# Kernel tuning notes

Measured on AMD Instinct MI355X. Metric: run time of the kernel, lower is better.

Reference implementation:

```python
import jax, jax.numpy as jnp
import numpy as np

EPS = 1e-5
H, DH = 8, 8  # n_head, d_hidden


def setup_inputs() -> dict:
    key = jax.random.key(0)
    ks = jax.random.split(key, 6)
    B, N, L, D = 1, 512, 1024, 64
    s = 1.0 / np.sqrt(D)
    return {
        "msa": jax.random.normal(ks[0], (B, N, L, D), jnp.float32),
        "ln_w": jnp.ones((D,), jnp.float32),
        "ln_b": jnp.zeros((D,), jnp.float32),
        "Wq": jax.random.normal(ks[1], (D, H * DH), jnp.float32) * s,
        "Wk": jax.random.normal(ks[2], (D, DH), jnp.float32) * s,
        "Wv": jax.random.normal(ks[3], (D, DH), jnp.float32) * s,
        "Wg": jax.random.normal(ks[4], (D, H * DH), jnp.float32) * s,
        "bg": jnp.ones((H * DH,), jnp.float32),
        "Wout": jax.random.normal(ks[5], (D, D), jnp.float32) * s,
        "bout": jnp.zeros((D,), jnp.float32),
    }


def reference(msa, ln_w, ln_b, Wq, Wk, Wv, Wg, bg, Wout, bout):
    B, N, L, D = msa.shape
    # LayerNorm over d_msa
    mu = jnp.mean(msa, axis=-1, keepdims=True)
    var = jnp.mean(jnp.square(msa - mu), axis=-1, keepdims=True)
    x = (msa - mu) * jax.lax.rsqrt(var + EPS) * ln_w + ln_b

    # Global query: project, split heads, mean over the N (sequence) axis
    q = (x @ Wq).reshape(B, N, L, H, DH).mean(axis=1)  # (B, L, H, DH)
    k = x @ Wk  # (B, N, L, DH)
    v = x @ Wv  # (B, N, L, DH)
    gate = jax.nn.sigmoid(x @ Wg + bg)  # (B, N, L, H*DH)

    scale = 1.0 / np.sqrt(DH)
    # SDPA batched over (B, L): q_len = H, kv_len = N, head_dim = DH
    scores = jnp.einsum("blhd,bnld->blhn", q, k) * scale
    attn = jax.nn.softmax(scores, axis=-1)
    o = jnp.einsum("blhn,bnld->blhd", attn, v)  # (B, L, H, DH)
    o = o.reshape(B, 1, L, H * DH)  # broadcast over N via gate

    out = (gate * o) @ Wout + bout  # (B, N, L, D)
    return out
```

## Files before the change

### kernel.cpp

```cpp
#include <hip/hip_runtime.h>
#include <math.h>

#define DD 64
#define NN 512
#define LL 1024
#define EPSF 1e-5f
#define NCH 32

typedef short short8 __attribute__((ext_vector_type(8)));
typedef float f32x4 __attribute__((ext_vector_type(4)));

static __device__ __forceinline__ unsigned bf16_rne(float f) {
  unsigned u = __float_as_uint(f);
  return (u + 0x7FFFu + ((u >> 16) & 1u)) >> 16;
}
static __device__ __forceinline__ float bf16_hi_f(float f) {
  unsigned u = __float_as_uint(f);
  return __uint_as_float((u + 0x7FFFu + ((u >> 16) & 1u)) & 0xFFFF0000u);
}

__global__ __launch_bounds__(256) void kW(const float* __restrict__ Wg,
                                          const float* __restrict__ Wout,
                                          unsigned* __restrict__ Bpk)
{
  const int idx = blockIdx.x * 256 + threadIdx.x;
  const int e2   = idx & 3;
  const int lane = (idx >> 2) & 63;
  const int ctkt = (idx >> 8) & 7;
  const int h    = (idx >> 11) & 1;
  const int mv   = (idx >> 12) & 1;
  const int col  = ((ctkt >> 1) << 4) | (lane & 15);
  const int k0   = ((ctkt & 1) << 5) + ((lane >> 4) << 3) + (e2 << 1);
  const float* W = mv ? Wout : Wg;
  const float w0 = W[k0 * DD + col];
  const float w1 = W[(k0 + 1) * DD + col];
  unsigned b0, b1;
  if (h == 0) { b0 = bf16_rne(w0); b1 = bf16_rne(w1); }
  else        { b0 = bf16_rne(w0 - bf16_hi_f(w0)); b1 = bf16_rne(w1 - bf16_hi_f(w1)); }
  Bpk[idx] = b0 | (b1 << 16);
}

__global__ __launch_bounds__(256, 4) void kA(
    const float* __restrict__ msa, const float* __restrict__ lnw, const float* __restrict__ lnb,
    const float* __restrict__ Wk, const float* __restrict__ Wv,
    float* __restrict__ kb, float* __restrict__ vb, float* __restrict__ xbarP,
    unsigned short* __restrict__ xnh)
{
  __shared__ float xc[4][16][68];
  const int t = threadIdx.x;
  const int lane = t & 63;
  const int w = t >> 6;
  const int l_loc = t & 15;
  const int n_loc = t >> 4;
  const int lt = blockIdx.x & 63;
  const int nc = blockIdx.x >> 6;
  const int l0 = lt * 16;
  const int n = nc * 16 + n_loc;
  const int l = l0 + l_loc;

  float X[DD];
  {
    const float4* rp = (const float4*)(msa + ((size_t)n * LL + l) * DD);
#pragma unroll
    for (int i = 0; i < 16; ++i) {
      const float4 f = rp[i];
      X[4*i+0] = f.x; X[4*i+1] = f.y; X[4*i+2] = f.z; X[4*i+3] = f.w;
    }
  }

  float s = 0.f, s2 = 0.f;
#pragma unroll
  for (int d = 0; d < DD; ++d) { s += X[d]; s2 = fmaf(X[d], X[d], s2); }
  const float mu = s * (1.f / DD);
  const float rs = rsqrtf(fmaf(-mu, mu, s2 * (1.f / DD)) + EPSF);
  const float aa = rs, bb = -mu * rs;

  float ka[8], va[8];
#pragma unroll
  for (int j = 0; j < 8; ++j) { ka[j] = 0.f; va[j] = 0.f; }

  uint4* xg = (uint4*)xnh;
#pragma unroll
  for (int g = 0; g < 8; ++g) {
#pragma unroll
    for (int e = 0; e < 8; ++e) {
      const int d = 8 * g + e;
      const float xn = fmaf(fmaf(X[d], aa, bb), lnw[d], lnb[d]);
      X[d] = xn;
#pragma unroll
      for (int j = 0; j < 8; ++j) {
        ka[j] = fmaf(xn, Wk[d * 8 + j], ka[j]);
        va[j] = fmaf(xn, Wv[d * 8 + j], va[j]);
      }
    }
    uint4 q;
    q.x = bf16_rne(X[8*g+0]) | (bf16_rne(X[8*g+1]) << 16);
    q.y = bf16_rne(X[8*g+2]) | (bf16_rne(X[8*g+3]) << 16);
    q.z = bf16_rne(X[8*g+4]) | (bf16_rne(X[8*g+5]) << 16);
    q.w = bf16_rne(X[8*g+6]) | (bf16_rne(X[8*g+7]) << 16);
    xg[(size_t)(n * 8 + g) * LL + l] = q;
  }

  {
    float4* kp = (float4*)(kb + ((size_t)l * NN + n) * 8);
    float4* vp = (float4*)(vb + ((size_t)l * NN + n) * 8);
    kp[0] = make_float4(ka[0], ka[1], ka[2], ka[3]);
    kp[1] = make_float4(ka[4], ka[5], ka[6], ka[7]);
    vp[0] = make_float4(va[0], va[1], va[2], va[3]);
    vp[1] = make_float4(va[4], va[5], va[6], va[7]);
  }

  {
    const bool hi1 = (lane & 16) != 0;
#pragma unroll
    for (int k = 0; k < 32; ++k) {
      const float keep = hi1 ? X[k + 32] : X[k];
      const float send = hi1 ? X[k] : X[k + 32];
      X[k] = keep + __shfl_xor(send, 16);
    }
    const bool hi2 = (lane & 32) != 0;
#pragma unroll
    for (int k = 0; k < 16; ++k) {
      const float keep = hi2 ? X[k + 16] : X[k];
      const float send = hi2 ? X[k] : X[k + 16];
      X[k] = keep + __shfl_xor(send, 32);
    }
  }
  const int d0i = ((lane >> 4) & 1) * 32 + (lane >> 5) * 16;
#pragma unroll
  for (int k = 0; k < 16; ++k) xc[w][l_loc][d0i + k] = X[k];
  __syncthreads();

#pragma unroll
  for (int j = 0; j < 4; ++j) {
    const int c = t * 4 + j;
    const int ll = c >> 6, d = c & 63;
    const float sv = xc[0][ll][d] + xc[1][ll][d] + xc[2][ll][d] + xc[3][ll][d];
    xbarP[((size_t)(l0 + ll) * NCH + nc) * DD + d] = sv;
  }
}

__global__ __launch_bounds__(512) void kB(
    const float* __restrict__ kb, const float* __restrict__ vb,
    const float* __restrict__ xbarP, const float* __restrict__ Wq,
    float* __restrict__ obT)
{
  __shared__ float xbL[DD];
  __shared__ float qs[DD];
  __shared__ float ks[NN * 9];
  __shared__ float vs[NN * 9];
  const int l = blockIdx.x;
  const int t = threadIdx.x;
  const int h = t >> 6;
  const int lane = t & 63;

  const float* kl = kb + (size_t)l * NN * 8;
  const float* vl = vb + (size_t)l * NN * 8;
#pragma unroll
  for (int i = 0; i < 8; ++i) {
    const int idx = i * 512 + t;
    const int n = idx >> 3, j = idx & 7;
    ks[n*9 + j] = kl[idx];
    vs[n*9 + j] = vl[idx];
  }
  if (t < DD) {
    float s = 0.f;
    for (int p = 0; p < NCH; ++p) s += xbarP[((size_t)l * NCH + p) * DD + t];
    xbL[t] = s * (1.f / NN);
  }
  __syncthreads();
  if (t < DD) {
    float acc = 0.f;
    for (int d = 0; d < DD; ++d) acc = fmaf(xbL[d], Wq[d*DD + t], acc);
    qs[t] = acc * 0.35355339059327373f;
  }
  __syncthreads();

  float sc[8];
  float m = -1e30f;
#pragma unroll
  for (int i = 0; i < 8; ++i) {
    const int n = i * 64 + lane;
    float s = 0.f;
#pragma unroll
    for (int d = 0; d < 8; ++d) s = fmaf(qs[h*8 + d], ks[n*9 + d], s);
    sc[i] = s;
    m = fmaxf(m, s);
  }
#pragma unroll
  for (int off = 32; off; off >>= 1) m = fmaxf(m, __shfl_xor(m, off));
  float ssum = 0.f;
#pragma unroll
  for (int i = 0; i < 8; ++i) { sc[i] = __expf(sc[i] - m); ssum += sc[i]; }
#pragma unroll
  for (int off = 32; off; off >>= 1) ssum += __shfl_xor(ssum, off);
  const float inv = 1.f / ssum;

  float oacc[8];
#pragma unroll
  for (int d = 0; d < 8; ++d) oacc[d] = 0.f;
#pragma unroll
  for (int i = 0; i < 8; ++i) {
    const int n = i * 64 + lane;
#pragma unroll
    for (int d = 0; d < 8; ++d) oacc[d] = fmaf(sc[i], vs[n*9 + d], oacc[d]);
  }
#pragma unroll
  for (int d = 0; d < 8; ++d) {
#pragma unroll
    for (int off = 32; off; off >>= 1) oacc[d] += __shfl_xor(oacc[d], off);
  }
  if (lane == 0) {
#pragma unroll
    for (int d = 0; d < 8; ++d)
      obT[(size_t)(h * 8 + d) * LL + l] = oacc[d] * inv;
  }
}

__global__ __launch_bounds__(256, 4) void kC(
    const unsigned short* __restrict__ xnh, const unsigned* __restrict__ Bpk,
    const float* __restrict__ bg, const float* __restrict__ obT,
    const float* __restrict__ bout, float* __restrict__ out)
{
  __shared__ unsigned short TH[128 * 72];
  __shared__ unsigned short TL[128 * 72];
  const int t = threadIdx.x;
  const int lane = t & 63;
  const int w = t >> 6;
  const int rbase = 32 * w;
  const size_t R0 = (size_t)blockIdx.x * 128;
  const int nblk = (int)(R0 >> 10);
  const int lbase = (int)(R0 & (LL - 1));

  const short8* Bp = (const short8*)Bpk;
  const short8* Xp = (const short8*)xnh;

  f32x4 acc[2][4];
#pragma unroll
  for (int rt = 0; rt < 2; ++rt)
#pragma unroll
    for (int ct = 0; ct < 4; ++ct) acc[rt][ct] = f32x4{0.f, 0.f, 0.f, 0.f};

  {
    short8 ah[2][2];
#pragma unroll
    for (int rt = 0; rt < 2; ++rt) {
      const int ar_l = lbase + rbase + rt * 16 + (lane & 15);
      const int g = lane >> 4;
      ah[rt][0] = Xp[(size_t)(nblk * 8 + g) * LL + ar_l];
      ah[rt][1] = Xp[(size_t)(nblk * 8 + 4 + g) * LL + ar_l];
    }
#pragma unroll
    for (int ct = 0; ct < 4; ++ct) {
      const short8 bh0 = Bp[(0 * 8 + ct * 2 + 0) * 64 + lane];
      const short8 bh1 = Bp[(0 * 8 + ct * 2 + 1) * 64 + lane];
      const short8 bl0 = Bp[(1 * 8 + ct * 2 + 0) * 64 + lane];
      const short8 bl1 = Bp[(1 * 8 + ct * 2 + 1) * 64 + lane];
#pragma unroll
      for (int rt = 0; rt < 2; ++rt) {
        f32x4 c = acc[rt][ct];
        c = __builtin_amdgcn_mfma_f32_16x16x32_bf16(ah[rt][0], bh0, c, 0, 0, 0);
        c = __builtin_amdgcn_mfma_f32_16x16x32_bf16(ah[rt][1], bh1, c, 0, 0, 0);
        c = __builtin_amdgcn_mfma_f32_16x16x32_bf16(ah[rt][0], bl0, c, 0, 0, 0);
        c = __builtin_amdgcn_mfma_f32_16x16x32_bf16(ah[rt][1], bl1, c, 0, 0, 0);
        acc[rt][ct] = c;
      }
    }
  }

#pragma unroll
  for (int rt = 0; rt < 2; ++rt) {
    const int rl0 = rbase + rt * 16 + ((lane >> 4) << 2);
    const int li0 = (int)((R0 + rl0) & (LL - 1));
#pragma unroll
    for (int ct = 0; ct < 4; ++ct) {
      const int col = ct * 16 + (lane & 15);
      const float4 ov = *(const float4*)&obT[(size_t)col * LL + li0];
      const float bgc = bg[col];
#define SIG_STORE(j, ocomp)                                             \
      {                                                                 \
        const float pre = acc[rt][ct][j] + bgc;                         \
        const float tv = (ocomp) / (1.f + __expf(-pre));                \
        const unsigned hb = bf16_rne(tv);                               \
        TH[(rl0 + (j)) * 72 + col] = (unsigned short)hb;                \
        const float rvl = tv - __uint_as_float(hb << 16);               \
        TL[(rl0 + (j)) * 72 + col] = (unsigned short)bf16_rne(rvl);     \
      }
      SIG_STORE(0, ov.x) SIG_STORE(1, ov.y) SIG_STORE(2, ov.z) SIG_STORE(3, ov.w)
#undef SIG_STORE
    }
  }

#pragma unroll
  for (int rt = 0; rt < 2; ++rt)
#pragma unroll
    for (int ct = 0; ct < 4; ++ct) {
      const float bo = bout[ct * 16 + (lane & 15)];
      acc[rt][ct] = f32x4{bo, bo, bo, bo};
    }
  {
    short8 ah[2][2], al[2][2];
#pragma unroll
    for (int rt = 0; rt < 2; ++rt) {
      const int ar = rbase + rt * 16 + (lane & 15);
      const int kg = (lane >> 4) * 8;
      ah[rt][0] = *(const short8*)&TH[ar * 72 + kg];
      ah[rt][1] = *(const short8*)&TH[ar * 72 + 32 + kg];
      al[rt][0] = *(const short8*)&TL[ar * 72 + kg];
      al[rt][1] = *(const short8*)&TL[ar * 72 + 32 + kg];
    }
#pragma unroll
    for (int ct = 0; ct < 4; ++ct) {
      const short8 bh0 = Bp[(2 * 8 + ct * 2 + 0) * 64 + lane];
      const short8 bh1 = Bp[(2 * 8 + ct * 2 + 1) * 64 + lane];
      const short8 bl0 = Bp[(3 * 8 + ct * 2 + 0) * 64 + lane];
      const short8 bl1 = Bp[(3 * 8 + ct * 2 + 1) * 64 + lane];
#pragma unroll
      for (int rt = 0; rt < 2; ++rt) {
        f32x4 c = acc[rt][ct];
        c = __builtin_amdgcn_mfma_f32_16x16x32_bf16(ah[rt][0], bh0, c, 0, 0, 0);
        c = __builtin_amdgcn_mfma_f32_16x16x32_bf16(ah[rt][1], bh1, c, 0, 0, 0);
        c = __builtin_amdgcn_mfma_f32_16x16x32_bf16(ah[rt][0], bl0, c, 0, 0, 0);
        c = __builtin_amdgcn_mfma_f32_16x16x32_bf16(ah[rt][1], bl1, c, 0, 0, 0);
        c = __builtin_amdgcn_mfma_f32_16x16x32_bf16(al[rt][0], bh0, c, 0, 0, 0);
        c = __builtin_amdgcn_mfma_f32_16x16x32_bf16(al[rt][1], bh1, c, 0, 0, 0);
        acc[rt][ct] = c;
      }
    }
  }

#pragma unroll
  for (int rt = 0; rt < 2; ++rt) {
#pragma unroll
    for (int j = 0; j < 4; ++j) {
      const size_t rg = R0 + rbase + rt * 16 + ((lane >> 4) << 2) + j;
#pragma unroll
      for (int ct = 0; ct < 4; ++ct)
        out[rg * DD + ct * 16 + (lane & 15)] = acc[rt][ct][j];
    }
  }
}

extern "C" void kernel_launch(void* const* d_in, const int* in_sizes, int n_in,
                              void* d_out, int out_size, void* d_ws, size_t ws_size,
                              hipStream_t stream)
{
  const float* msa  = (const float*)d_in[0];
  const float* lnw  = (const float*)d_in[1];
  const float* lnb  = (const float*)d_in[2];
  const float* Wq   = (const float*)d_in[3];
  const float* Wk   = (const float*)d_in[4];
  const float* Wv   = (const float*)d_in[5];
  const float* Wg   = (const float*)d_in[6];
  const float* bg   = (const float*)d_in[7];
  const float* Wout = (const float*)d_in[8];
  const float* bout = (const float*)d_in[9];
  float* out = (float*)d_out;

  float* kb    = (float*)d_ws;
  float* vb    = kb + (size_t)LL * NN * 8;
  float* xbarP = vb + (size_t)LL * NN * 8;
  float* obT   = xbarP + (size_t)LL * NCH * DD;
  unsigned* Bpk = (unsigned*)(obT + (size_t)DD * LL);
  unsigned short* xnh = (unsigned short*)(Bpk + 8192);

  kW<<<32, 256, 0, stream>>>(Wg, Wout, Bpk);
  kA<<<64 * NCH, 256, 0, stream>>>(msa, lnw, lnb, Wk, Wv, kb, vb, xbarP, xnh);
  kB<<<LL, 512, 0, stream>>>(kb, vb, xbarP, Wq, obT);
  kC<<<(NN * LL) / 128, 256, 0, stream>>>(xnh, Bpk, bg, obT, bout, out);
}
```

Baseline: 128.4 us.

## Recompute LayerNorm in output GEMM from msa and stats instead of storing bf16 x

The stats kernel no longer writes the normalized activations as bf16. It stores only per-row scale and shift values. The gate/output GEMM kernel re-reads fp32 msa, applies the LayerNorm on the fly and packs it to bf16 fragments. This removes a large intermediate write, but kC now reads fp32 input, which is twice the bytes of the bf16 buffer.

```diff
diff --git a/kernel.cpp b/kernel.cpp
--- a/kernel.cpp
+++ b/kernel.cpp
@@ -17,6 +17,12 @@
 static __device__ __forceinline__ float bf16_hi_f(float f) {
   unsigned u = __float_as_uint(f);
   return __uint_as_float((u + 0x7FFFu + ((u >> 16) & 1u)) & 0xFFFF0000u);
+}
+static __device__ __forceinline__ short8 pack8(unsigned a, unsigned b,
+                                               unsigned c, unsigned d) {
+  union { uint4 u; short8 s; } x;
+  x.u = make_uint4(a, b, c, d);
+  return x.s;
 }
 
 __global__ __launch_bounds__(256) void kW(const float* __restrict__ Wg,
@@ -44,7 +50,7 @@
     const float* __restrict__ msa, const float* __restrict__ lnw, const float* __restrict__ lnb,
     const float* __restrict__ Wk, const float* __restrict__ Wv,
     float* __restrict__ kb, float* __restrict__ vb, float* __restrict__ xbarP,
-    unsigned short* __restrict__ xnh)
+    float* __restrict__ stats)
 {
   __shared__ float xc[4][16][68];
   const int t = threadIdx.x;
@@ -73,32 +79,24 @@
   for (int d = 0; d < DD; ++d) { s += X[d]; s2 = fmaf(X[d], X[d], s2); }
   const float mu = s * (1.f / DD);
   const float rs = rsqrtf(fmaf(-mu, mu, s2 * (1.f / DD)) + EPSF);
-  const float aa = rs, bb = -mu * rs;
+
+  {
+    float2* sp = (float2*)(stats + ((size_t)n * LL + l) * 2);
+    *sp = make_float2(rs, -mu * rs);
+  }
 
   float ka[8], va[8];
 #pragma unroll
   for (int j = 0; j < 8; ++j) { ka[j] = 0.f; va[j] = 0.f; }
-
-  uint4* xg = (uint4*)xnh;
-#pragma unroll
-  for (int g = 0; g < 8; ++g) {
-#pragma unroll
-    for (int e = 0; e < 8; ++e) {
-      const int d = 8 * g + e;
-      const float xn = fmaf(fmaf(X[d], aa, bb), lnw[d], lnb[d]);
-      X[d] = xn;
-#pragma unroll
-      for (int j = 0; j < 8; ++j) {
-        ka[j] = fmaf(xn, Wk[d * 8 + j], ka[j]);
-        va[j] = fmaf(xn, Wv[d * 8 + j], va[j]);
-      }
-    }
-    uint4 q;
-    q.x = bf16_rne(X[8*g+0]) | (bf16_rne(X[8*g+1]) << 16);
-    q.y = bf16_rne(X[8*g+2]) | (bf16_rne(X[8*g+3]) << 16);
-    q.z = bf16_rne(X[8*g+4]) | (bf16_rne(X[8*g+5]) << 16);
-    q.w = bf16_rne(X[8*g+6]) | (bf16_rne(X[8*g+7]) << 16);
-    xg[(size_t)(n * 8 + g) * LL + l] = q;
+#pragma unroll
+  for (int d = 0; d < DD; ++d) {
+    const float xn = fmaf((X[d] - mu) * rs, lnw[d], lnb[d]);
+    X[d] = xn;
+#pragma unroll
+    for (int j = 0; j < 8; ++j) {
+      ka[j] = fmaf(xn, Wk[d * 8 + j], ka[j]);
+      va[j] = fmaf(xn, Wv[d * 8 + j], va[j]);
+    }
   }
 
   {
@@ -218,9 +216,11 @@
 }
 
 __global__ __launch_bounds__(256, 4) void kC(
-    const unsigned short* __restrict__ xnh, const unsigned* __restrict__ Bpk,
-    const float* __restrict__ bg, const float* __restrict__ obT,
-    const float* __restrict__ bout, float* __restrict__ out)
+    const float* __restrict__ msa, const float* __restrict__ stats,
+    const float* __restrict__ lnw, const float* __restrict__ lnb,
+    const unsigned* __restrict__ Bpk, const float* __restrict__ bg,
+    const float* __restrict__ obT, const float* __restrict__ bout,
+    float* __restrict__ out)
 {
   __shared__ unsigned short TH[128 * 72];
   __shared__ unsigned short TL[128 * 72];
@@ -229,11 +229,8 @@
   const int w = t >> 6;
   const int rbase = 32 * w;
   const size_t R0 = (size_t)blockIdx.x * 128;
-  const int nblk = (int)(R0 >> 10);
-  const int lbase = (int)(R0 & (LL - 1));
 
   const short8* Bp = (const short8*)Bpk;
-  const short8* Xp = (const short8*)xnh;
 
   f32x4 acc[2][4];
 #pragma unroll
@@ -245,10 +242,29 @@
     short8 ah[2][2];
 #pragma unroll
     for (int rt = 0; rt < 2; ++rt) {
-      const int ar_l = lbase + rbase + rt * 16 + (lane & 15);
-      const int g = lane >> 4;
-      ah[rt][0] = Xp[(size_t)(nblk * 8 + g) * LL + ar_l];
-      ah[rt][1] = Xp[(size_t)(nblk * 8 + 4 + g) * LL + ar_l];
+      const size_t ar = R0 + rbase + rt * 16 + (lane & 15);
+      const int kg = (lane >> 4) * 8;
+      const float2 ab = *(const float2*)&stats[ar * 2];
+      const float aa = ab.x, bb = ab.y;
+#pragma unroll
+      for (int hh = 0; hh < 2; ++hh) {
+        const int d0 = kg + hh * 32;
+        const float4 f0 = *(const float4*)&msa[ar * DD + d0];
+        const float4 f1 = *(const float4*)&msa[ar * DD + d0 + 4];
+        const float4 w0 = *(const float4*)&lnw[d0];
+        const float4 w1 = *(const float4*)&lnw[d0 + 4];
+        const float4 b0 = *(const float4*)&lnb[d0];
+        const float4 b1 = *(const float4*)&lnb[d0 + 4];
+        const unsigned q0 = bf16_rne(fmaf(fmaf(f0.x, aa, bb), w0.x, b0.x)) |
+                           (bf16_rne(fmaf(fmaf(f0.y, aa, bb), w0.y, b0.y)) << 16);
+        const unsigned q1 = bf16_rne(fmaf(fmaf(f0.z, aa, bb), w0.z, b0.z)) |
+                           (bf16_rne(fmaf(fmaf(f0.w, aa, bb), w0.w, b0.w)) << 16);
+        const unsigned q2 = bf16_rne(fmaf(fmaf(f1.x, aa, bb), w1.x, b1.x)) |
+                           (bf16_rne(fmaf(fmaf(f1.y, aa, bb), w1.y, b1.y)) << 16);
+        const unsigned q3 = bf16_rne(fmaf(fmaf(f1.z, aa, bb), w1.z, b1.z)) |
+                           (bf16_rne(fmaf(fmaf(f1.w, aa, bb), w1.w, b1.w)) << 16);
+        ah[rt][hh] = pack8(q0, q1, q2, q3);
+      }
     }
 #pragma unroll
     for (int ct = 0; ct < 4; ++ct) {
@@ -362,10 +378,10 @@
   float* xbarP = vb + (size_t)LL * NN * 8;
   float* obT   = xbarP + (size_t)LL * NCH * DD;
   unsigned* Bpk = (unsigned*)(obT + (size_t)DD * LL);
-  unsigned short* xnh = (unsigned short*)(Bpk + 8192);
+  float* stats = (float*)(Bpk + 8192);
 
   kW<<<32, 256, 0, stream>>>(Wg, Wout, Bpk);
-  kA<<<64 * NCH, 256, 0, stream>>>(msa, lnw, lnb, Wk, Wv, kb, vb, xbarP, xnh);
+  kA<<<64 * NCH, 256, 0, stream>>>(msa, lnw, lnb, Wk, Wv, kb, vb, xbarP, stats);
   kB<<<LL, 512, 0, stream>>>(kb, vb, xbarP, Wq, obT);
-  kC<<<(NN * LL) / 128, 256, 0, stream>>>(xnh, Bpk, bg, obT, bout, out);
-}
+  kC<<<(NN * LL) / 128, 256, 0, stream>>>(msa, stats, lnw, lnb, Bpk, bg, obT, bout, out);
+}
```

Measured after the change: 125.9 us. Within noise of the previous version (-1.9%).
